# Performance work log

Hardware: AMD Instinct MI355X
Metric: run time of the kernel (lower is better)

Reference implementation:

```python
import jax, jax.numpy as jnp
import numpy as np

N_NODES = 50000
N_EDGES = 800000
HID = 128
EDGE_FEAT = 4
NUM_G = 20
R_MIN, R_MAX = 0.0, 100.0  # r_max = 10.0**2


def _mlp2(x, w1, b1, w2, b2, act_last):
    y = jax.nn.relu(x @ w1 + b1)
    y = y @ w2 + b2
    return jax.nn.relu(y) if act_last else y


def _linear_init(key, fan_in, fan_out):
    kw, kb = jax.random.split(key)
    lim = 1.0 / np.sqrt(fan_in)
    w = jax.random.uniform(kw, (fan_in, fan_out), jnp.float32, -lim, lim)
    b = jax.random.uniform(kb, (fan_out,), jnp.float32, -lim, lim)
    return w, b


def setup_inputs():
    key = jax.random.key(0)
    ks = jax.random.split(key, 16)
    src = jax.random.randint(ks[0], (N_EDGES,), 0, N_NODES)
    dst = jax.random.randint(ks[1], (N_EDGES,), 0, N_NODES)
    edge_feat = jax.random.normal(ks[2], (N_EDGES, EDGE_FEAT), jnp.float32)
    h = jax.random.normal(ks[3], (N_NODES, HID), jnp.float32)
    x = jax.random.normal(ks[4], (N_NODES, 3), jnp.float32)
    ein = 2 * HID + EDGE_FEAT + NUM_G
    ew1, eb1 = _linear_init(ks[5], ein, HID)
    ew2, eb2 = _linear_init(ks[6], HID, HID)
    infw, infb = _linear_init(ks[7], HID, 1)
    xw1, xb1 = _linear_init(ks[8], HID, HID)
    xw2, xb2 = _linear_init(ks[9], HID, 1)
    nw1, nb1 = _linear_init(ks[10], 2 * HID, HID)
    nw2, nb2 = _linear_init(ks[11], HID, HID)
    return {"src": src, "dst": dst, "edge_feat": edge_feat, "h": h, "x": x,
            "ew1": ew1, "eb1": eb1, "ew2": ew2, "eb2": eb2,
            "infw": infw, "infb": infb,
            "xw1": xw1, "xb1": xb1, "xw2": xw2, "xb2": xb2,
            "nw1": nw1, "nb1": nb1, "nw2": nw2, "nb2": nb2}


def reference(src, dst, edge_feat, h, x,
              ew1, eb1, ew2, eb2, infw, infb,
              xw1, xb1, xw2, xb2, nw1, nb1, nw2, nb2):
    n_nodes = h.shape[0]
    rel_x = x[dst] - x[src]                      # [E, 3]
    r = jnp.sum(rel_x * rel_x, -1, keepdims=True)  # [E, 1]
    # GaussianSmearing expansion
    offsets = jnp.linspace(R_MIN, R_MAX, NUM_G)
    coeff = -0.5 / (offsets[1] - offsets[0]) ** 2
    r_feat = jnp.exp(coeff * (r - offsets) ** 2)  # [E, NUM_G]
    # edge message MLP (act_last=True)
    cat = jnp.concatenate([edge_feat, r_feat, h[dst], h[src]], axis=-1)
    mij = _mlp2(cat, ew1, eb1, ew2, eb2, act_last=True)  # [E, HID]
    eij = jax.nn.sigmoid(mij @ infw + infb)              # [E, 1]
    mi = jax.ops.segment_sum(mij * eij, dst, num_segments=n_nodes)  # [N, HID]
    h_new = h + _mlp2(jnp.concatenate([mi, h], -1), nw1, nb1, nw2, nb2, act_last=False)
    # coordinate update: (xi - xj) == rel_x
    x_scale = _mlp2(mij, xw1, xb1, xw2, xb2, act_last=False)  # [E, 1]
    delta_x = jax.ops.segment_sum(rel_x * x_scale, dst, num_segments=n_nodes)
    x_new = x + delta_x
    return h_new, x_new
```

## Files before the change

### kernel.cpp

```cpp
#include <hip/hip_runtime.h>

#define HID 128
#define NNODES 50000
#define NEDGES 800000

typedef __attribute__((ext_vector_type(8))) short short8;
typedef __attribute__((ext_vector_type(4))) float f32x4;

union U8 { short8 v; unsigned short u[8]; };

__device__ __forceinline__ unsigned short f2b(float f) {
  unsigned int u = __float_as_uint(f);
  u += 0x7FFFu + ((u >> 16) & 1u);
  return (unsigned short)(u >> 16);
}

__device__ __forceinline__ unsigned int pk2(float a, float b) {
  unsigned int ua = __float_as_uint(a);
  ua += 0x7FFFu + ((ua >> 16) & 1u);
  unsigned int ub = __float_as_uint(b);
  ub += 0x7FFFu + ((ub >> 16) & 1u);
  return (ua >> 16) | (ub & 0xFFFF0000u);
}

__device__ __forceinline__ unsigned int pk2h(float a, float b) {
  unsigned int ua = __float_as_uint(a) + 0x8000u;
  unsigned int ub = __float_as_uint(b) + 0x8000u;
  return (ua >> 16) | (ub & 0xFFFF0000u);
}

__device__ __forceinline__ void atomicPkAddBf16(unsigned short* addr, unsigned int packed) {
  asm volatile("global_atomic_pk_add_bf16 %0, %1, off" :: "v"(addr), "v"(packed) : "memory");
}

__device__ __forceinline__ int stage_chunk(int c0, int row) {
  return ((c0 >> 3) ^ (row & 7) ^ (((row >> 2) & 3) << 1)) & 15;
}

__global__ __launch_bounds__(256) void pack_kernel(
    const float* __restrict__ ew1, const float* __restrict__ ew2,
    const float* __restrict__ xw1, const float* __restrict__ nw1,
    const float* __restrict__ nw2, unsigned short* __restrict__ ws) {
  int i = blockIdx.x * 256 + threadIdx.x;
  const float* w; int base, ksrc;
  if (i < 36864)       { w = ew1; base = 0;      ksrc = 280; }
  else if (i < 53248)  { w = ew2; base = 36864;  ksrc = 128; }
  else if (i < 69632)  { w = xw1; base = 53248;  ksrc = 128; }
  else if (i < 102400) { w = nw1; base = 69632;  ksrc = 256; }
  else if (i < 118784) { w = nw2; base = 102400; ksrc = 128; }
  else return;
  int li = i - base;
  int j = li & 7, t = li >> 3;
  int col = t & 127, kg = t >> 7;
  int k = kg * 8 + j;
  float v = (k < ksrc) ? w[k * 128 + col] : 0.0f;
  ws[i] = f2b(v);
}

__global__ __launch_bounds__(256) void hpack_kernel(
    const float* __restrict__ h, unsigned short* __restrict__ hB) {
  int i = blockIdx.x * 256 + threadIdx.x;
  const float4* p = reinterpret_cast<const float4*>(h + (size_t)i * 8);
  float4 a = p[0], b = p[1];
  uint4 u;
  u.x = pk2(a.x, a.y); u.y = pk2(a.z, a.w);
  u.z = pk2(b.x, b.y); u.w = pk2(b.z, b.w);
  *reinterpret_cast<uint4*>(hB + (size_t)i * 8) = u;
}

template<int MODE>
__global__ __launch_bounds__(256, 4) void edge_kernel(
    const int* __restrict__ src, const int* __restrict__ dst,
    const float* __restrict__ ef, const float* __restrict__ h,
    const float* __restrict__ x,
    const float* __restrict__ eb1, const float* __restrict__ eb2,
    const float* __restrict__ infw, const float* __restrict__ infb,
    const float* __restrict__ xb1, const float* __restrict__ xw2,
    const float* __restrict__ xb2,
    const short8* __restrict__ W1p, const short8* __restrict__ W2p,
    const short8* __restrict__ XW1p,
    const unsigned short* __restrict__ hB,
    float* __restrict__ miF, unsigned short* __restrict__ miB,
    float* __restrict__ dx) {
  __shared__ __align__(16) char catB[64 * 576];
  __shared__ int dL[64], sL[64];
  __shared__ float relL[64][3];
  __shared__ float ppart[4][64];
  __shared__ float eijL[64];

  const int tid = threadIdx.x;
  const int e0 = blockIdx.x * 64;
  const int lane = tid & 63, w = tid >> 6;
  const int lr = lane & 15, lg = lane >> 4;
  const int l7 = lr & 7, l3 = lr & 3;
  const int colb = w*32 + lr;

  {
    int row = tid >> 2, sub = tid & 3;
    int e = e0 + row;
    int s = src[e], d = dst[e];
    if (sub == 0) { sL[row] = s; dL[row] = d; }
    float rx = x[3*d+0] - x[3*s+0];
    float ry = x[3*d+1] - x[3*s+1];
    float rz = x[3*d+2] - x[3*s+2];
    if (sub == 1) { relL[row][0] = rx; relL[row][1] = ry; relL[row][2] = rz; }
    float r = rx*rx + ry*ry + rz*rz;
    const float step = 100.0f / 19.0f;
    const float co = -0.5f / (step * step);
    float v6[6];
    if (sub == 0) {
      const float4 efv = reinterpret_cast<const float4*>(ef)[e];
      v6[0]=efv.x; v6[1]=efv.y; v6[2]=efv.z; v6[3]=efv.w;
      float t1 = r - step;
      v6[4] = __expf(co * r * r);
      v6[5] = __expf(co * t1 * t1);
    } else {
      #pragma unroll
      for (int q = 0; q < 6; ++q) {
        float g = (float)(sub*6 - 4 + q) * step;
        float t = r - g;
        v6[q] = __expf(co * t * t);
      }
    }
    #pragma unroll
    for (int q = 0; q < 3; ++q) {
      int c = sub*6 + q*2;
      int chunk = (c>>3) ^ (row&7);
      *reinterpret_cast<unsigned int*>(catB + row*576 + (chunk<<4) + ((c&7)<<1)) = pk2h(v6[q*2], v6[q*2+1]);
    }
    if (sub == 3) {
      U8 z;
      #pragma unroll
      for (int j = 0; j < 8; ++j) z.u[j] = 0;
      *reinterpret_cast<short8*>(catB + row*576 + ((32 + (3 ^ (row&3)))<<4)) = z.v;
    }
  }

  #pragma unroll
  for (int it = 0; it < 8; ++it) {
    int i = tid + it*256;
    int row = i >> 5, c = i & 31;
    int node = (c < 16) ? dst[e0+row] : src[e0+row];
    int chunk = 3 + c;
    int sw = (chunk < 32) ? (chunk ^ (row&7)) : (32 + ((chunk&3) ^ (row&3)));
    if (MODE == 2) {
      short8 u = *reinterpret_cast<const short8*>(hB + (size_t)node*128 + (c&15)*8);
      *reinterpret_cast<short8*>(catB + row*576 + (sw<<4)) = u;
    } else {
      const float4* hp = reinterpret_cast<const float4*>(h + (size_t)node*128 + (c&15)*8);
      float4 a = hp[0], b = hp[1];
      uint4 u;
      u.x = pk2(a.x, a.y); u.y = pk2(a.z, a.w);
      u.z = pk2(b.x, b.y); u.w = pk2(b.z, b.w);
      *reinterpret_cast<uint4*>(catB + row*576 + (sw<<4)) = u;
    }
  }

  short8 p00 = W1p[(0*4+lg)*128 + colb], p01 = W1p[(0*4+lg)*128 + colb + 16];
  short8 p10 = W1p[(1*4+lg)*128 + colb], p11 = W1p[(1*4+lg)*128 + colb + 16];
  __syncthreads();

  f32x4 acc[4][2];
  #pragma unroll
  for (int t = 0; t < 4; ++t) { acc[t][0] = (f32x4)0.0f; acc[t][1] = (f32x4)0.0f; }
  #pragma unroll
  for (int kt = 0; kt < 9; ++kt) {
    int ch = (kt < 8) ? ((kt*4+lg) ^ l7) : (32 + (lg ^ l3));
    short8 a0 = *reinterpret_cast<const short8*>(catB + (0*16+lr)*576 + (ch<<4));
    short8 a1 = *reinterpret_cast<const short8*>(catB + (1*16+lr)*576 + (ch<<4));
    short8 a2 = *reinterpret_cast<const short8*>(catB + (2*16+lr)*576 + (ch<<4));
    short8 a3 = *reinterpret_cast<const short8*>(catB + (3*16+lr)*576 + (ch<<4));
    short8 b0, b1;
    if (kt == 0)      { b0 = p00; b1 = p01; }
    else if (kt == 1) { b0 = p10; b1 = p11; }
    else              { b0 = W1p[(kt*4+lg)*128 + colb]; b1 = W1p[(kt*4+lg)*128 + colb + 16]; }
    acc[0][0] = __builtin_amdgcn_mfma_f32_16x16x32_bf16(b0, a0, acc[0][0], 0, 0, 0);
    acc[0][1] = __builtin_amdgcn_mfma_f32_16x16x32_bf16(b1, a0, acc[0][1], 0, 0, 0);
    acc[1][0] = __builtin_amdgcn_mfma_f32_16x16x32_bf16(b0, a1, acc[1][0], 0, 0, 0);
    acc[1][1] = __builtin_amdgcn_mfma_f32_16x16x32_bf16(b1, a1, acc[1][1], 0, 0, 0);
    acc[2][0] = __builtin_amdgcn_mfma_f32_16x16x32_bf16(b0, a2, acc[2][0], 0, 0, 0);
    acc[2][1] = __builtin_amdgcn_mfma_f32_16x16x32_bf16(b1, a2, acc[2][1], 0, 0, 0);
    acc[3][0] = __builtin_amdgcn_mfma_f32_16x16x32_bf16(b0, a3, acc[3][0], 0, 0, 0);
    acc[3][1] = __builtin_amdgcn_mfma_f32_16x16x32_bf16(b1, a3, acc[3][1], 0, 0, 0);
  }
  __syncthreads();

  {
    const int c00 = w*32 + lg*4, c01 = c00 + 16;
    float4 be0 = *reinterpret_cast<const float4*>(eb1 + c00);
    float4 be1 = *reinterpret_cast<const float4*>(eb1 + c01);
    #pragma unroll
    for (int t = 0; t < 4; ++t) {
      int row = t*16 + lr;
      char* rowB = catB + row*576;
      #pragma unroll
      for (int j = 0; j < 2; ++j) {
        const float4 be = j ? be1 : be0;
        int c0 = j ? c01 : c00;
        float v0 = fmaxf(acc[t][j][0] + be.x, 0.f);
        float v1 = fmaxf(acc[t][j][1] + be.y, 0.f);
        float v2 = fmaxf(acc[t][j][2] + be.z, 0.f);
        float v3 = fmaxf(acc[t][j][3] + be.w, 0.f);
        uint2 pv; pv.x = pk2h(v0, v1); pv.y = pk2h(v2, v3);
        int chunk = (c0>>3) ^ (row&7);
        *reinterpret_cast<uint2*>(rowB + (chunk<<4) + ((c0&7)<<1)) = pv;
      }
    }
  }
  __syncthreads();

  f32x4 acc2[4][2];
  #pragma unroll
  for (int t = 0; t < 4; ++t) { acc2[t][0] = (f32x4)0.0f; acc2[t][1] = (f32x4)0.0f; }
  #pragma unroll
  for (int kt = 0; kt < 4; ++kt) {
    int ch = (kt*4+lg) ^ l7;
    short8 a0 = *reinterpret_cast<const short8*>(catB + (0*16+lr)*576 + (ch<<4));
    short8 a1 = *reinterpret_cast<const short8*>(catB + (1*16+lr)*576 + (ch<<4));
    short8 a2 = *reinterpret_cast<const short8*>(catB + (2*16+lr)*576 + (ch<<4));
    short8 a3 = *reinterpret_cast<const short8*>(catB + (3*16+lr)*576 + (ch<<4));
    short8 b0 = W2p[(kt*4+lg)*128 + colb];
    short8 b1 = W2p[(kt*4+lg)*128 + colb + 16];
    acc2[0][0] = __builtin_amdgcn_mfma_f32_16x16x32_bf16(b0, a0, acc2[0][0], 0, 0, 0);
    acc2[0][1] = __builtin_amdgcn_mfma_f32_16x16x32_bf16(b1, a0, acc2[0][1], 0, 0, 0);
    acc2[1][0] = __builtin_amdgcn_mfma_f32_16x16x32_bf16(b0, a1, acc2[1][0], 0, 0, 0);
    acc2[1][1] = __builtin_amdgcn_mfma_f32_16x16x32_bf16(b1, a1, acc2[1][1], 0, 0, 0);
    acc2[2][0] = __builtin_amdgcn_mfma_f32_16x16x32_bf16(b0, a2, acc2[2][0], 0, 0, 0);
    acc2[2][1] = __builtin_amdgcn_mfma_f32_16x16x32_bf16(b1, a2, acc2[2][1], 0, 0, 0);
    acc2[3][0] = __builtin_amdgcn_mfma_f32_16x16x32_bf16(b0, a3, acc2[3][0], 0, 0, 0);
    acc2[3][1] = __builtin_amdgcn_mfma_f32_16x16x32_bf16(b1, a3, acc2[3][1], 0, 0, 0);
  }
  float pl[4];
  {
    const int c00 = w*32 + lg*4, c01 = c00 + 16;
    float4 be0 = *reinterpret_cast<const float4*>(eb2 + c00);
    float4 be1 = *reinterpret_cast<const float4*>(eb2 + c01);
    float4 iw0 = *reinterpret_cast<const float4*>(infw + c00);
    float4 iw1 = *reinterpret_cast<const float4*>(infw + c01);
    #pragma unroll
    for (int t = 0; t < 4; ++t) {
      int row = t*16 + lr;
      char* rowB = catB + row*576;
      pl[t] = 0.f;
      #pragma unroll
      for (int j = 0; j < 2; ++j) {
        const float4 be = j ? be1 : be0;
        const float4 iw = j ? iw1 : iw0;
        int c0 = j ? c01 : c00;
        float v0 = fmaxf(acc2[t][j][0] + be.x, 0.f);
        float v1 = fmaxf(acc2[t][j][1] + be.y, 0.f);
        float v2 = fmaxf(acc2[t][j][2] + be.z, 0.f);
        float v3 = fmaxf(acc2[t][j][3] + be.w, 0.f);
        acc2[t][j][0] = v0; acc2[t][j][1] = v1; acc2[t][j][2] = v2; acc2[t][j][3] = v3;
        pl[t] += v0*iw.x + v1*iw.y + v2*iw.z + v3*iw.w;
        uint2 pv; pv.x = pk2h(v0, v1); pv.y = pk2h(v2, v3);
        int chunk = 16 + ((c0>>3) ^ (row&7));
        *reinterpret_cast<uint2*>(rowB + (chunk<<4) + ((c0&7)<<1)) = pv;
      }
    }
    #pragma unroll
    for (int t = 0; t < 4; ++t) {
      pl[t] += __shfl_xor(pl[t], 16, 64);
      pl[t] += __shfl_xor(pl[t], 32, 64);
    }
    if (lane < 16) {
      #pragma unroll
      for (int t = 0; t < 4; ++t) ppart[w][t*16 + lane] = pl[t];
    }
  }
  __syncthreads();

  if (lane < 16) {
    int row2 = w*16 + lane;
    float s2 = ppart[0][row2] + ppart[1][row2] + ppart[2][row2] + ppart[3][row2] + infb[0];
    eijL[row2] = 1.f / (1.f + __expf(-s2));
  }
  __syncthreads();

  if (MODE >= 1) {
    const int c00 = w*32 + lg*4, c01 = c00 + 16;
    #pragma unroll
    for (int t = 0; t < 4; ++t) {
      int row = t*16 + lr;
      float e = eijL[row];
      char* rowB = catB + row*576;
      #pragma unroll
      for (int j = 0; j < 2; ++j) {
        int c0 = j ? c01 : c00;
        uint2 pv;
        pv.x = pk2h(acc2[t][j][0]*e, acc2[t][j][1]*e);
        pv.y = pk2h(acc2[t][j][2]*e, acc2[t][j][3]*e);
        *reinterpret_cast<uint2*>(rowB + (stage_chunk(c0, row)<<4) + ((c0&7)<<1)) = pv;
      }
    }
  } else {
    const int c00 = w*32 + lg*4, c01 = c00 + 16;
    #pragma unroll
    for (int t = 0; t < 4; ++t) {
      int row = t*16 + lr;
      int d = dL[row];
      float e = eijL[row];
      float* fp = miF + (size_t)d*128;
      #pragma unroll
      for (int j = 0; j < 2; ++j) {
        int c0 = j ? c01 : c00;
        #pragma unroll
        for (int rg = 0; rg < 4; ++rg) atomicAdd(fp + c0 + rg, acc2[t][j][rg]*e);
      }
    }
  }
  __syncthreads();

  if (MODE >= 1) {
    #pragma unroll
    for (int t = 0; t < 4; ++t)
      #pragma unroll
      for (int rg = 0; rg < 4; ++rg) {
        int row = t*16 + lg*4 + rg;
        int d = dL[row];
        int col0 = w*32 + lr*2;
        unsigned int val = *reinterpret_cast<const unsigned int*>(
            catB + row*576 + (stage_chunk(col0, row)<<4) + ((col0&7)<<1));
        if (val) atomicPkAddBf16(miB + (size_t)d*128 + col0, val);
      }
  }

  f32x4 acc3[4][2];
  #pragma unroll
  for (int t = 0; t < 4; ++t) { acc3[t][0] = (f32x4)0.0f; acc3[t][1] = (f32x4)0.0f; }
  #pragma unroll
  for (int kt = 0; kt < 4; ++kt) {
    int ch = 16 + ((kt*4+lg) ^ l7);
    short8 a0 = *reinterpret_cast<const short8*>(catB + (0*16+lr)*576 + (ch<<4));
    short8 a1 = *reinterpret_cast<const short8*>(catB + (1*16+lr)*576 + (ch<<4));
    short8 a2 = *reinterpret_cast<const short8*>(catB + (2*16+lr)*576 + (ch<<4));
    short8 a3 = *reinterpret_cast<const short8*>(catB + (3*16+lr)*576 + (ch<<4));
    short8 b0 = XW1p[(kt*4+lg)*128 + colb];
    short8 b1 = XW1p[(kt*4+lg)*128 + colb + 16];
    acc3[0][0] = __builtin_amdgcn_mfma_f32_16x16x32_bf16(b0, a0, acc3[0][0], 0, 0, 0);
    acc3[0][1] = __builtin_amdgcn_mfma_f32_16x16x32_bf16(b1, a0, acc3[0][1], 0, 0, 0);
    acc3[1][0] = __builtin_amdgcn_mfma_f32_16x16x32_bf16(b0, a1, acc3[1][0], 0, 0, 0);
    acc3[1][1] = __builtin_amdgcn_mfma_f32_16x16x32_bf16(b1, a1, acc3[1][1], 0, 0, 0);
    acc3[2][0] = __builtin_amdgcn_mfma_f32_16x16x32_bf16(b0, a2, acc3[2][0], 0, 0, 0);
    acc3[2][1] = __builtin_amdgcn_mfma_f32_16x16x32_bf16(b1, a2, acc3[2][1], 0, 0, 0);
    acc3[3][0] = __builtin_amdgcn_mfma_f32_16x16x32_bf16(b0, a3, acc3[3][0], 0, 0, 0);
    acc3[3][1] = __builtin_amdgcn_mfma_f32_16x16x32_bf16(b1, a3, acc3[3][1], 0, 0, 0);
  }

  {
    const int c00 = w*32 + lg*4, c01 = c00 + 16;
    float4 bx0 = *reinterpret_cast<const float4*>(xb1 + c00);
    float4 bx1 = *reinterpret_cast<const float4*>(xb1 + c01);
    float4 xw0 = *reinterpret_cast<const float4*>(xw2 + c00);
    float4 xw1v = *reinterpret_cast<const float4*>(xw2 + c01);
    float ql[4];
    #pragma unroll
    for (int t = 0; t < 4; ++t) {
      ql[t] = 0.f;
      #pragma unroll
      for (int j = 0; j < 2; ++j) {
        const float4 bx = j ? bx1 : bx0;
        const float4 xw = j ? xw1v : xw0;
        ql[t] += fmaxf(acc3[t][j][0] + bx.x, 0.f) * xw.x
               + fmaxf(acc3[t][j][1] + bx.y, 0.f) * xw.y
               + fmaxf(acc3[t][j][2] + bx.z, 0.f) * xw.z
               + fmaxf(acc3[t][j][3] + bx.w, 0.f) * xw.w;
      }
      ql[t] += __shfl_xor(ql[t], 16, 64);
      ql[t] += __shfl_xor(ql[t], 32, 64);
    }
    if (lane < 16) {
      #pragma unroll
      for (int t = 0; t < 4; ++t) ppart[w][t*16 + lane] = ql[t];
    }
  }
  __syncthreads();

  if (tid < 192) {
    int row = tid / 3, c = tid - row*3;
    float q = ppart[0][row] + ppart[1][row] + ppart[2][row] + ppart[3][row] + xb2[0];
    atomicAdd(dx + dL[row]*3 + c, relL[row][c] * q);
  }
}

template<int MODE>
__global__ __launch_bounds__(256) void node_kernel(
    const float* __restrict__ h, const float* __restrict__ x,
    const float* __restrict__ nb1, const float* __restrict__ nb2,
    const short8* __restrict__ NW1p, const short8* __restrict__ NW2p,
    const unsigned short* __restrict__ miB,
    const unsigned short* __restrict__ hB,
    float* __restrict__ out) {
  __shared__ __align__(16) char c2B[64 * 512];
  __shared__ __align__(16) char y3B[64 * 256];
  const int tid = threadIdx.x;
  const int n0 = blockIdx.x * 64;
  const float* mi = out;

  for (int i = tid; i < 64*32; i += 256) {
    int row = i >> 5, c = i & 31;
    int node = n0 + row;
    U8 u;
    if (node < NNODES) {
      if (c < 16 && MODE >= 1) {
        u.v = *reinterpret_cast<const short8*>(miB + (size_t)node*128 + c*8);
      } else if (c >= 16 && MODE == 2) {
        u.v = *reinterpret_cast<const short8*>(hB + (size_t)node*128 + (c-16)*8);
      } else {
        const float4* p = (c < 16)
          ? reinterpret_cast<const float4*>(mi + (size_t)node*128 + c*8)
          : reinterpret_cast<const float4*>(h + (size_t)node*128 + (c-16)*8);
        float4 a = p[0], b = p[1];
        uint4 uu;
        uu.x = pk2(a.x, a.y); uu.y = pk2(a.z, a.w);
        uu.z = pk2(b.x, b.y); uu.w = pk2(b.z, b.w);
        u.v = *reinterpret_cast<short8*>(&uu);
      }
    } else {
      #pragma unroll
      for (int j = 0; j < 8; ++j) u.u[j] = 0;
    }
    *reinterpret_cast<short8*>(c2B + row*512 + ((c ^ (row&7))<<4)) = u.v;
  }
  __syncthreads();

  const int lane = tid & 63, wave = tid >> 6;
  const int lr = lane & 15, lg = lane >> 4;
  const int rb = wave * 16;
  const int arow = rb + lr;

  f32x4 acc[8];
  #pragma unroll
  for (int nt = 0; nt < 8; ++nt) acc[nt] = (f32x4)0.0f;
  #pragma unroll
  for (int kt = 0; kt < 8; ++kt) {
    int chunk = kt*4 + lg;
    short8 a = *reinterpret_cast<const short8*>(c2B + arow*512 + ((chunk ^ (arow&7))<<4));
    const short8* bp = NW1p + chunk*128 + lr;
    #pragma unroll
    for (int nt = 0; nt < 8; ++nt)
      acc[nt] = __builtin_amdgcn_mfma_f32_16x16x32_bf16(a, bp[nt*16], acc[nt], 0, 0, 0);
  }
  #pragma unroll
  for (int nt = 0; nt < 8; ++nt) {
    int col = nt*16 + lr;
    float bias = nb1[col];
    #pragma unroll
    for (int r = 0; r < 4; ++r) {
      int row = rb + lg*4 + r;
      float v = fmaxf(acc[nt][r] + bias, 0.f);
      *reinterpret_cast<unsigned short*>(y3B + row*256 + (((col>>3) ^ (row&7))<<4) + ((col&7)<<1)) = f2b(v);
    }
  }

  f32x4 acc2[8];
  #pragma unroll
  for (int nt = 0; nt < 8; ++nt) acc2[nt] = (f32x4)0.0f;
  #pragma unroll
  for (int kt = 0; kt < 4; ++kt) {
    int chunk = kt*4 + lg;
    short8 a = *reinterpret_cast<const short8*>(y3B + arow*256 + ((chunk ^ (arow&7))<<4));
    const short8* bp = NW2p + chunk*128 + lr;
    #pragma unroll
    for (int nt = 0; nt < 8; ++nt)
      acc2[nt] = __builtin_amdgcn_mfma_f32_16x16x32_bf16(a, bp[nt*16], acc2[nt], 0, 0, 0);
  }
  __syncthreads();
  #pragma unroll
  for (int nt = 0; nt < 8; ++nt) {
    int col = nt*16 + lr;
    float b2 = nb2[col];
    #pragma unroll
    for (int r = 0; r < 4; ++r) {
      int row = rb + lg*4 + r;
      int node = n0 + row;
      if (node < NNODES) {
        int idx = node*128 + col;
        out[idx] = acc2[nt][r] + b2 + h[idx];
      }
    }
  }

  if (tid < 192) {
    int node = n0 + tid/3;
    if (node < NNODES) {
      int idx = node*3 + (tid%3);
      float* xo = out + NNODES*HID;
      xo[idx] = x[idx] + xo[idx];
    }
  }
}

extern "C" void kernel_launch(void* const* d_in, const int* in_sizes, int n_in,
                              void* d_out, int out_size, void* d_ws, size_t ws_size,
                              hipStream_t stream) {
  const int*   src  = (const int*)  d_in[0];
  const int*   dst  = (const int*)  d_in[1];
  const float* ef   = (const float*)d_in[2];
  const float* h    = (const float*)d_in[3];
  const float* x    = (const float*)d_in[4];
  const float* ew1  = (const float*)d_in[5];
  const float* eb1  = (const float*)d_in[6];
  const float* ew2  = (const float*)d_in[7];
  const float* eb2  = (const float*)d_in[8];
  const float* infw = (const float*)d_in[9];
  const float* infb = (const float*)d_in[10];
  const float* xw1  = (const float*)d_in[11];
  const float* xb1  = (const float*)d_in[12];
  const float* xw2  = (const float*)d_in[13];
  const float* xb2  = (const float*)d_in[14];
  const float* nw1  = (const float*)d_in[15];
  const float* nb1  = (const float*)d_in[16];
  const float* nw2  = (const float*)d_in[17];
  const float* nb2  = (const float*)d_in[18];

  float* out = (float*)d_out;
  float* miF = out;
  float* dxp = out + NNODES*HID;
  unsigned short* wsp = (unsigned short*)d_ws;
  unsigned short* miB = wsp + 118784;
  unsigned short* hBp = miB + (size_t)NNODES*HID;

  const size_t MIN = (size_t)NNODES*HID;
  size_t need1 = (118784u + MIN) * 2u;
  size_t need2 = (118784u + 2u*MIN) * 2u;
  int mode = (ws_size >= need2) ? 2 : (ws_size >= need1 ? 1 : 0);

  if (mode >= 1) {
    hipMemsetAsync(miB, 0, MIN*2, stream);
    hipMemsetAsync(dxp, 0, (size_t)NNODES*3*4, stream);
  } else {
    hipMemsetAsync(d_out, 0, (size_t)out_size * sizeof(float), stream);
  }

  pack_kernel<<<464, 256, 0, stream>>>(ew1, ew2, xw1, nw1, nw2, wsp);
  if (mode == 2) hpack_kernel<<<(NNODES*HID)/(256*8), 256, 0, stream>>>(h, hBp);

  if (mode == 2) {
    edge_kernel<2><<<NEDGES/64, 256, 0, stream>>>(
        src, dst, ef, h, x, eb1, eb2, infw, infb, xb1, xw2, xb2,
        (const short8*)wsp, (const short8*)(wsp + 36864), (const short8*)(wsp + 53248),
        hBp, miF, miB, dxp);
    node_kernel<2><<<(NNODES + 63)/64, 256, 0, stream>>>(
        h, x, nb1, nb2,
        (const short8*)(wsp + 69632), (const short8*)(wsp + 102400), miB, hBp, out);
  } else if (mode == 1) {
    edge_kernel<1><<<NEDGES/64, 256, 0, stream>>>(
        src, dst, ef, h, x, eb1, eb2, infw, infb, xb1, xw2, xb2,
        (const short8*)wsp, (const short8*)(wsp + 36864), (const short8*)(wsp + 53248),
        hBp, miF, miB, dxp);
    node_kernel<1><<<(NNODES + 63)/64, 256, 0, stream>>>(
        h, x, nb1, nb2,
        (const short8*)(wsp + 69632), (const short8*)(wsp + 102400), miB, hBp, out);
  } else {
    edge_kernel<0><<<NEDGES/64, 256, 0, stream>>>(
        src, dst, ef, h, x, eb1, eb2, infw, infb, xb1, xw2, xb2,
        (const short8*)wsp, (const short8*)(wsp + 36864), (const short8*)(wsp + 53248),
        hBp, miF, miB, dxp);
    node_kernel<0><<<(NNODES + 63)/64, 256, 0, stream>>>(
        h, x, nb1, nb2,
        (const short8*)(wsp + 69632), (const short8*)(wsp + 102400), miB, hBp, out);
  }
}
```

Before: 314.4 us.

## Process 128 edges per block with 512 threads in edge kernel

Doubles the edge tile per block to 128 edges, using 8 waves split into two row groups by four column groups. Each wave still computes a 64x32 output tile, but weight fragments and per-block setup are shared across more edges and fewer blocks launch. This adds LDS usage per block and heavier barriers, and the launch bound hint may tighten register allocation.

```diff
diff --git a/kernel.cpp b/kernel.cpp
--- a/kernel.cpp
+++ b/kernel.cpp
@@ -3,6 +3,7 @@
 #define HID 128
 #define NNODES 50000
 #define NEDGES 800000
+#define EPB 128
 
 typedef __attribute__((ext_vector_type(8))) short short8;
 typedef __attribute__((ext_vector_type(4))) float f32x4;
@@ -69,7 +70,7 @@
 }
 
 template<int MODE>
-__global__ __launch_bounds__(256, 4) void edge_kernel(
+__global__ __launch_bounds__(512, 4) void edge_kernel(
     const int* __restrict__ src, const int* __restrict__ dst,
     const float* __restrict__ ef, const float* __restrict__ h,
     const float* __restrict__ x,
@@ -82,18 +83,21 @@
     const unsigned short* __restrict__ hB,
     float* __restrict__ miF, unsigned short* __restrict__ miB,
     float* __restrict__ dx) {
-  __shared__ __align__(16) char catB[64 * 576];
-  __shared__ int dL[64], sL[64];
-  __shared__ float relL[64][3];
-  __shared__ float ppart[4][64];
-  __shared__ float eijL[64];
+  __shared__ __align__(16) char catB[EPB * 576];
+  __shared__ int dL[EPB], sL[EPB];
+  __shared__ float relL[EPB][3];
+  __shared__ float ppart[8][EPB];
+  __shared__ float eijL[EPB];
 
   const int tid = threadIdx.x;
-  const int e0 = blockIdx.x * 64;
+  const int e0 = blockIdx.x * EPB;
   const int lane = tid & 63, w = tid >> 6;
+  const int wm = w >> 2, wn = w & 3;
   const int lr = lane & 15, lg = lane >> 4;
   const int l7 = lr & 7, l3 = lr & 3;
-  const int colb = w*32 + lr;
+  const int colb = wn*32 + lr;
+  const int c00 = wn*32 + lg*4, c01 = c00 + 16;
+  const int rbase = wm*64;
 
   {
     int row = tid >> 2, sub = tid & 3;
@@ -138,7 +142,7 @@
 
   #pragma unroll
   for (int it = 0; it < 8; ++it) {
-    int i = tid + it*256;
+    int i = tid + it*512;
     int row = i >> 5, c = i & 31;
     int node = (c < 16) ? dst[e0+row] : src[e0+row];
     int chunk = 3 + c;
@@ -166,32 +170,25 @@
   #pragma unroll
   for (int kt = 0; kt < 9; ++kt) {
     int ch = (kt < 8) ? ((kt*4+lg) ^ l7) : (32 + (lg ^ l3));
-    short8 a0 = *reinterpret_cast<const short8*>(catB + (0*16+lr)*576 + (ch<<4));
-    short8 a1 = *reinterpret_cast<const short8*>(catB + (1*16+lr)*576 + (ch<<4));
-    short8 a2 = *reinterpret_cast<const short8*>(catB + (2*16+lr)*576 + (ch<<4));
-    short8 a3 = *reinterpret_cast<const short8*>(catB + (3*16+lr)*576 + (ch<<4));
     short8 b0, b1;
     if (kt == 0)      { b0 = p00; b1 = p01; }
     else if (kt == 1) { b0 = p10; b1 = p11; }
     else              { b0 = W1p[(kt*4+lg)*128 + colb]; b1 = W1p[(kt*4+lg)*128 + colb + 16]; }
-    acc[0][0] = __builtin_amdgcn_mfma_f32_16x16x32_bf16(b0, a0, acc[0][0], 0, 0, 0);
-    acc[0][1] = __builtin_amdgcn_mfma_f32_16x16x32_bf16(b1, a0, acc[0][1], 0, 0, 0);
-    acc[1][0] = __builtin_amdgcn_mfma_f32_16x16x32_bf16(b0, a1, acc[1][0], 0, 0, 0);
-    acc[1][1] = __builtin_amdgcn_mfma_f32_16x16x32_bf16(b1, a1, acc[1][1], 0, 0, 0);
-    acc[2][0] = __builtin_amdgcn_mfma_f32_16x16x32_bf16(b0, a2, acc[2][0], 0, 0, 0);
-    acc[2][1] = __builtin_amdgcn_mfma_f32_16x16x32_bf16(b1, a2, acc[2][1], 0, 0, 0);
-    acc[3][0] = __builtin_amdgcn_mfma_f32_16x16x32_bf16(b0, a3, acc[3][0], 0, 0, 0);
-    acc[3][1] = __builtin_amdgcn_mfma_f32_16x16x32_bf16(b1, a3, acc[3][1], 0, 0, 0);
+    #pragma unroll
+    for (int t = 0; t < 4; ++t) {
+      short8 a = *reinterpret_cast<const short8*>(catB + (rbase + t*16 + lr)*576 + (ch<<4));
+      acc[t][0] = __builtin_amdgcn_mfma_f32_16x16x32_bf16(b0, a, acc[t][0], 0, 0, 0);
+      acc[t][1] = __builtin_amdgcn_mfma_f32_16x16x32_bf16(b1, a, acc[t][1], 0, 0, 0);
+    }
   }
   __syncthreads();
 
   {
-    const int c00 = w*32 + lg*4, c01 = c00 + 16;
     float4 be0 = *reinterpret_cast<const float4*>(eb1 + c00);
     float4 be1 = *reinterpret_cast<const float4*>(eb1 + c01);
     #pragma unroll
     for (int t = 0; t < 4; ++t) {
-      int row = t*16 + lr;
+      int row = rbase + t*16 + lr;
       char* rowB = catB + row*576;
       #pragma unroll
       for (int j = 0; j < 2; ++j) {
@@ -215,31 +212,24 @@
   #pragma unroll
   for (int kt = 0; kt < 4; ++kt) {
     int ch = (kt*4+lg) ^ l7;
-    short8 a0 = *reinterpret_cast<const short8*>(catB + (0*16+lr)*576 + (ch<<4));
-    short8 a1 = *reinterpret_cast<const short8*>(catB + (1*16+lr)*576 + (ch<<4));
-    short8 a2 = *reinterpret_cast<const short8*>(catB + (2*16+lr)*576 + (ch<<4));
-    short8 a3 = *reinterpret_cast<const short8*>(catB + (3*16+lr)*576 + (ch<<4));
     short8 b0 = W2p[(kt*4+lg)*128 + colb];
     short8 b1 = W2p[(kt*4+lg)*128 + colb + 16];
-    acc2[0][0] = __builtin_amdgcn_mfma_f32_16x16x32_bf16(b0, a0, acc2[0][0], 0, 0, 0);
-    acc2[0][1] = __builtin_amdgcn_mfma_f32_16x16x32_bf16(b1, a0, acc2[0][1], 0, 0, 0);
-    acc2[1][0] = __builtin_amdgcn_mfma_f32_16x16x32_bf16(b0, a1, acc2[1][0], 0, 0, 0);
-    acc2[1][1] = __builtin_amdgcn_mfma_f32_16x16x32_bf16(b1, a1, acc2[1][1], 0, 0, 0);
-    acc2[2][0] = __builtin_amdgcn_mfma_f32_16x16x32_bf16(b0, a2, acc2[2][0], 0, 0, 0);
-    acc2[2][1] = __builtin_amdgcn_mfma_f32_16x16x32_bf16(b1, a2, acc2[2][1], 0, 0, 0);
-    acc2[3][0] = __builtin_amdgcn_mfma_f32_16x16x32_bf16(b0, a3, acc2[3][0], 0, 0, 0);
-    acc2[3][1] = __builtin_amdgcn_mfma_f32_16x16x32_bf16(b1, a3, acc2[3][1], 0, 0, 0);
-  }
-  float pl[4];
+    #pragma unroll
+    for (int t = 0; t < 4; ++t) {
+      short8 a = *reinterpret_cast<const short8*>(catB + (rbase + t*16 + lr)*576 + (ch<<4));
+      acc2[t][0] = __builtin_amdgcn_mfma_f32_16x16x32_bf16(b0, a, acc2[t][0], 0, 0, 0);
+      acc2[t][1] = __builtin_amdgcn_mfma_f32_16x16x32_bf16(b1, a, acc2[t][1], 0, 0, 0);
+    }
+  }
   {
-    const int c00 = w*32 + lg*4, c01 = c00 + 16;
     float4 be0 = *reinterpret_cast<const float4*>(eb2 + c00);
     float4 be1 = *reinterpret_cast<const float4*>(eb2 + c01);
     float4 iw0 = *reinterpret_cast<const float4*>(infw + c00);
     float4 iw1 = *reinterpret_cast<const float4*>(infw + c01);
-    #pragma unroll
-    for (int t = 0; t < 4; ++t) {
-      int row = t*16 + lr;
+    float pl[4];
+    #pragma unroll
+    for (int t = 0; t < 4; ++t) {
+      int row = rbase + t*16 + lr;
       char* rowB = catB + row*576;
       pl[t] = 0.f;
       #pragma unroll
@@ -251,7 +241,7 @@
         float v1 = fmaxf(acc2[t][j][1] + be.y, 0.f);
         float v2 = fmaxf(acc2[t][j][2] + be.z, 0.f);
         float v3 = fmaxf(acc2[t][j][3] + be.w, 0.f);
-        acc2[t][j][0] = v0; acc2[t][j][1] = v1; acc2[t][j][2] = v2; acc2[t][j][3] = v3;
+        acc2[t][j][0]=v0; acc2[t][j][1]=v1; acc2[t][j][2]=v2; acc2[t][j][3]=v3;
         pl[t] += v0*iw.x + v1*iw.y + v2*iw.z + v3*iw.w;
         uint2 pv; pv.x = pk2h(v0, v1); pv.y = pk2h(v2, v3);
         int chunk = 16 + ((c0>>3) ^ (row&7));
@@ -265,23 +255,23 @@
     }
     if (lane < 16) {
       #pragma unroll
-      for (int t = 0; t < 4; ++t) ppart[w][t*16 + lane] = pl[t];
-    }
-  }
-  __syncthreads();
-
-  if (lane < 16) {
-    int row2 = w*16 + lane;
-    float s2 = ppart[0][row2] + ppart[1][row2] + ppart[2][row2] + ppart[3][row2] + infb[0];
-    eijL[row2] = 1.f / (1.f + __expf(-s2));
+      for (int t = 0; t < 4; ++t) ppart[w][rbase + t*16 + lane] = pl[t];
+    }
+  }
+  __syncthreads();
+
+  if (tid < EPB) {
+    int wmr = tid >> 6;
+    float s2 = infb[0] + ppart[wmr*4+0][tid] + ppart[wmr*4+1][tid]
+                       + ppart[wmr*4+2][tid] + ppart[wmr*4+3][tid];
+    eijL[tid] = 1.f / (1.f + __expf(-s2));
   }
   __syncthreads();
 
   if (MODE >= 1) {
-    const int c00 = w*32 + lg*4, c01 = c00 + 16;
-    #pragma unroll
-    for (int t = 0; t < 4; ++t) {
-      int row = t*16 + lr;
+    #pragma unroll
+    for (int t = 0; t < 4; ++t) {
+      int row = rbase + t*16 + lr;
       float e = eijL[row];
       char* rowB = catB + row*576;
       #pragma unroll
@@ -294,10 +284,9 @@
       }
     }
   } else {
-    const int c00 = w*32 + lg*4, c01 = c00 + 16;
-    #pragma unroll
-    for (int t = 0; t < 4; ++t) {
-      int row = t*16 + lr;
+    #pragma unroll
+    for (int t = 0; t < 4; ++t) {
+      int row = rbase + t*16 + lr;
       int d = dL[row];
       float e = eijL[row];
       float* fp = miF + (size_t)d*128;
@@ -312,17 +301,15 @@
   __syncthreads();
 
   if (MODE >= 1) {
-    #pragma unroll
-    for (int t = 0; t < 4; ++t)
-      #pragma unroll
-      for (int rg = 0; rg < 4; ++rg) {
-        int row = t*16 + lg*4 + rg;
-        int d = dL[row];
-        int col0 = w*32 + lr*2;
-        unsigned int val = *reinterpret_cast<const unsigned int*>(
-            catB + row*576 + (stage_chunk(col0, row)<<4) + ((col0&7)<<1));
-        if (val) atomicPkAddBf16(miB + (size_t)d*128 + col0, val);
-      }
+    int col0 = wn*32 + lr*2;
+    #pragma unroll
+    for (int t2 = 0; t2 < 16; ++t2) {
+      int row = rbase + t2*4 + lg;
+      int d = dL[row];
+      unsigned int val = *reinterpret_cast<const unsigned int*>(
+          catB + row*576 + (stage_chunk(col0, row)<<4) + ((col0&7)<<1));
+      if (val) atomicPkAddBf16(miB + (size_t)d*128 + col0, val);
+    }
   }
 
   f32x4 acc3[4][2];
@@ -331,24 +318,16 @@
   #pragma unroll
   for (int kt = 0; kt < 4; ++kt) {
     int ch = 16 + ((kt*4+lg) ^ l7);
-    short8 a0 = *reinterpret_cast<const short8*>(catB + (0*16+lr)*576 + (ch<<4));
-    short8 a1 = *reinterpret_cast<const short8*>(catB + (1*16+lr)*576 + (ch<<4));
-    short8 a2 = *reinterpret_cast<const short8*>(catB + (2*16+lr)*576 + (ch<<4));
-    short8 a3 = *reinterpret_cast<const short8*>(catB + (3*16+lr)*576 + (ch<<4));
     short8 b0 = XW1p[(kt*4+lg)*128 + colb];
     short8 b1 = XW1p[(kt*4+lg)*128 + colb + 16];
-    acc3[0][0] = __builtin_amdgcn_mfma_f32_16x16x32_bf16(b0, a0, acc3[0][0], 0, 0, 0);
-    acc3[0][1] = __builtin_amdgcn_mfma_f32_16x16x32_bf16(b1, a0, acc3[0][1], 0, 0, 0);
-    acc3[1][0] = __builtin_amdgcn_mfma_f32_16x16x32_bf16(b0, a1, acc3[1][0], 0, 0, 0);
-    acc3[1][1] = __builtin_amdgcn_mfma_f32_16x16x32_bf16(b1, a1, acc3[1][1], 0, 0, 0);
-    acc3[2][0] = __builtin_amdgcn_mfma_f32_16x16x32_bf16(b0, a2, acc3[2][0], 0, 0, 0);
-    acc3[2][1] = __builtin_amdgcn_mfma_f32_16x16x32_bf16(b1, a2, acc3[2][1], 0, 0, 0);
-    acc3[3][0] = __builtin_amdgcn_mfma_f32_16x16x32_bf16(b0, a3, acc3[3][0], 0, 0, 0);
-    acc3[3][1] = __builtin_amdgcn_mfma_f32_16x16x32_bf16(b1, a3, acc3[3][1], 0, 0, 0);
-  }
-
+    #pragma unroll
+    for (int t = 0; t < 4; ++t) {
+      short8 a = *reinterpret_cast<const short8*>(catB + (rbase + t*16 + lr)*576 + (ch<<4));
+      acc3[t][0] = __builtin_amdgcn_mfma_f32_16x16x32_bf16(b0, a, acc3[t][0], 0, 0, 0);
+      acc3[t][1] = __builtin_amdgcn_mfma_f32_16x16x32_bf16(b1, a, acc3[t][1], 0, 0, 0);
+    }
+  }
   {
-    const int c00 = w*32 + lg*4, c01 = c00 + 16;
     float4 bx0 = *reinterpret_cast<const float4*>(xb1 + c00);
     float4 bx1 = *reinterpret_cast<const float4*>(xb1 + c01);
     float4 xw0 = *reinterpret_cast<const float4*>(xw2 + c00);
@@ -371,14 +350,16 @@
     }
     if (lane < 16) {
       #pragma unroll
-      for (int t = 0; t < 4; ++t) ppart[w][t*16 + lane] = ql[t];
-    }
-  }
-  __syncthreads();
-
-  if (tid < 192) {
+      for (int t = 0; t < 4; ++t) ppart[w][rbase + t*16 + lane] = ql[t];
+    }
+  }
+  __syncthreads();
+
+  if (tid < EPB*3) {
     int row = tid / 3, c = tid - row*3;
-    float q = ppart[0][row] + ppart[1][row] + ppart[2][row] + ppart[3][row] + xb2[0];
+    int wmr = row >> 6;
+    float q = xb2[0] + ppart[wmr*4+0][row] + ppart[wmr*4+1][row]
+                     + ppart[wmr*4+2][row] + ppart[wmr*4+3][row];
     atomicAdd(dx + dL[row]*3 + c, relL[row][c] * q);
   }
 }
@@ -537,7 +518,7 @@
   if (mode == 2) hpack_kernel<<<(NNODES*HID)/(256*8), 256, 0, stream>>>(h, hBp);
 
   if (mode == 2) {
-    edge_kernel<2><<<NEDGES/64, 256, 0, stream>>>(
+    edge_kernel<2><<<NEDGES/EPB, 512, 0, stream>>>(
         src, dst, ef, h, x, eb1, eb2, infw, infb, xb1, xw2, xb2,
         (const short8*)wsp, (const short8*)(wsp + 36864), (const short8*)(wsp + 53248),
         hBp, miF, miB, dxp);
@@ -545,7 +526,7 @@
         h, x, nb1, nb2,
         (const short8*)(wsp + 69632), (const short8*)(wsp + 102400), miB, hBp, out);
   } else if (mode == 1) {
-    edge_kernel<1><<<NEDGES/64, 256, 0, stream>>>(
+    edge_kernel<1><<<NEDGES/EPB, 512, 0, stream>>>(
         src, dst, ef, h, x, eb1, eb2, infw, infb, xb1, xw2, xb2,
         (const short8*)wsp, (const short8*)(wsp + 36864), (const short8*)(wsp + 53248),
         hBp, miF, miB, dxp);
@@ -553,7 +534,7 @@
         h, x, nb1, nb2,
         (const short8*)(wsp + 69632), (const short8*)(wsp + 102400), miB, hBp, out);
   } else {
-    edge_kernel<0><<<NEDGES/64, 256, 0, stream>>>(
+    edge_kernel<0><<<NEDGES/EPB, 512, 0, stream>>>(
         src, dst, ef, h, x, eb1, eb2, infw, infb, xb1, xw2, xb2,
         (const short8*)wsp, (const short8*)(wsp + 36864), (const short8*)(wsp + 53248),
         hBp, miF, miB, dxp);
```

Result: slower. 328.3 us (+4.4%).
